# Optimization experiments

Hardware: AMD Instinct MI355X
Metric: run time of the kernel (lower is better)

## Reference

```python
import jax, jax.numpy as jnp
import numpy as np

B, S, D = 4, 2048, 1024


def setup_inputs() -> dict:
    key = jax.random.key(0)
    k1, k2, k3 = jax.random.split(key, 3)
    x = jax.random.normal(k1, (B, S, D), dtype=jnp.float32)
    # torch nn.Linear weights are [out_features, in_features]
    wq_w = jax.random.normal(k2, (D, D), dtype=jnp.float32) * (1.0 / np.sqrt(D))
    wv_w = jax.random.normal(k3, (D, D), dtype=jnp.float32) * (1.0 / np.sqrt(D))
    return {"x": x, "wq_w": wq_w, "wv_w": wv_w}


def reference(x, wq_w, wv_w):
    b, s, d = x.shape
    q = x @ wq_w.T                      # [B,S,D]
    kv = x @ wv_w.T                     # [B,S,D]  (original uses wv for BOTH k and v; wk unused)
    # original: k.view(B, k_dim, -1) -- a raw memory RESHAPE, not a transpose
    k_r = kv.reshape(b, d, s)           # [B,D,S]
    scores = jnp.einsum('bsd,bdt->bst', q, k_r) / np.sqrt(d)  # [B,S,S]
    sm = jax.nn.softmax(scores, axis=-1)
    sm = jnp.tril(sm)                   # post-softmax causal mask (rows NOT renormalized)
    return jnp.einsum('bst,btd->bsd', sm, kv)
```

## Files before the change

kernel.cpp:

```cpp
#include <hip/hip_runtime.h>


typedef __attribute__((ext_vector_type(8))) _Float16 f16x8;
typedef __attribute__((ext_vector_type(4))) _Float16 f16x4;
typedef __attribute__((ext_vector_type(4))) float f32x4;

__device__ __forceinline__ void glds16(const void* g, void* l) {
  __builtin_amdgcn_global_load_lds((const __attribute__((address_space(1))) void*)g,
                                   (__attribute__((address_space(3))) void*)l, 16, 0, 0);
}
#define BAR() __builtin_amdgcn_s_barrier()
#define LGKM0() do { asm volatile("s_waitcnt lgkmcnt(0)" ::: "memory"); \
                     __builtin_amdgcn_sched_barrier(0); } while (0)
#define VM2() asm volatile("s_waitcnt vmcnt(2)" ::: "memory")
#define VM0() asm volatile("s_waitcnt vmcnt(0)" ::: "memory")
#define PR1() __builtin_amdgcn_s_setprio(1)
#define PR0() __builtin_amdgcn_s_setprio(0)

__device__ __forceinline__ unsigned pkh2(float a, float b) {
  union { _Float16 h[2]; unsigned u; } c;
  c.h[0] = (_Float16)a; c.h[1] = (_Float16)b;
  return c.u;
}

__global__ __launch_bounds__(256) void cvt3(const float* __restrict__ x,
                                            const float* __restrict__ wq,
                                            const float* __restrict__ wv,
                                            _Float16* __restrict__ xh,
                                            _Float16* __restrict__ wqh,
                                            _Float16* __restrict__ wvh) {
  int i = blockIdx.x * 256 + threadIdx.x;
  const float* src;
  _Float16* dst;
  int off;
  if (i < 2097152) { src = x; dst = xh; off = i; }
  else if (i < 2359296) { src = wq; dst = wqh; off = i - 2097152; }
  else { src = wv; dst = wvh; off = i - 2359296; }
  float4 v = ((const float4*)src)[off];
  f16x4 o = {(_Float16)v.x, (_Float16)v.y, (_Float16)v.z, (_Float16)v.w};
  ((f16x4*)dst)[off] = o;
}

template <typename OUT_T, int EPI>
__global__ __launch_bounds__(512, 2) void gemm8p(const _Float16* __restrict__ A,
                                                 const _Float16* __restrict__ BT,
                                                 OUT_T* __restrict__ C,
                                                 _Float16* __restrict__ T1,
                                                 _Float16* __restrict__ T2,
                                                 int K, int ldc,
                                                 long sA, long sB, long sC, float scale,
                                                 int lgx, int lgy) {
  extern __shared__ char smem[];
  _Float16* lds = (_Float16*)smem;
  const int lin = blockIdx.x + gridDim.x * (blockIdx.y + gridDim.y * blockIdx.z);
  const int xcd = lin & 7, s = lin >> 3;
  const int G = (gridDim.y * gridDim.z) >> 3;
  const int mx = s & ((1 << lgx) - 1);
  const int pid = xcd * G + (s >> lgx);
  const int ny = pid & (gridDim.y - 1);
  const int bz = pid >> lgy;
  A += (size_t)bz * sA;
  BT += (size_t)bz * sB;
  C += (size_t)bz * sC;
  const int m0 = mx << 8, n0 = ny << 8;
  const int tid = threadIdx.x, lane = tid & 63, wave = tid >> 6;
  const int wm = wave >> 2, wn = wave & 3;
  const int lr = lane & 15, lk = lane >> 4, xr = lane & 7;
  const int nkt = K >> 6;
  const int A0 = 0, A1 = 8192, B0 = 16384, B1 = 24576, BUF = 32768;
  const int baseA = wm ? A1 : A0;
  const int baseB = B0 + ((wn >> 1) << 13);
  const int bRow = (wn & 1) << 6;
  const int srow = lane >> 3;
  const int scolB = ((lane & 7) << 4) ^ (srow << 4);

  f32x4 acc[8][4] = {};
  f16x8 fa[4][2], fb[4][2];

#define STAGE(bufsel, halfsel, G_, hrow0, kt) do {                                   \
    const _Float16* _g = (G_) + (size_t)((hrow0) + wave * 16 + srow) * K + ((kt) << 6); \
    glds16((const char*)_g + scolB, (char*)&lds[(bufsel) * BUF + (halfsel) + wave * 1024]); \
    glds16((const char*)(_g + (size_t)8 * K) + scolB,                                \
           (char*)&lds[(bufsel) * BUF + (halfsel) + wave * 1024 + 512]);             \
  } while (0)
#define RDA(buf, mf, ks) (*(const f16x8*)&lds[(buf) * BUF + baseA + ((mf) * 16 + lr) * 64 + \
                                              ((((ks) * 4 + lk) ^ xr) << 3)])
#define RDB(buf, nf, ks) (*(const f16x8*)&lds[(buf) * BUF + baseB + (bRow + (nf) * 16 + lr) * 64 + \
                                              ((((ks) * 4 + lk) ^ xr) << 3)])
#define RDFA4(b, mbase) do { _Pragma("unroll")                                        \
    for (int i = 0; i < 4; ++i) { fa[i][0] = RDA(b, (mbase) + i, 0);                  \
                                  fa[i][1] = RDA(b, (mbase) + i, 1); } } while (0)
#define RDFB2(b, jbase) do { _Pragma("unroll")                                        \
    for (int j = 0; j < 2; ++j) { fb[(jbase) + j][0] = RDB(b, (jbase) + j, 0);        \
                                  fb[(jbase) + j][1] = RDB(b, (jbase) + j, 1); } } while (0)
#define MMQ(ib, jb) do { _Pragma("unroll")                                            \
    for (int i = 0; i < 4; ++i) { _Pragma("unroll")                                   \
      for (int j = 0; j < 2; ++j) {                                                   \
        acc[(ib) + i][(jb) + j] = __builtin_amdgcn_mfma_f32_16x16x32_f16(             \
            fa[i][0], fb[(jb) + j][0], acc[(ib) + i][(jb) + j], 0, 0, 0);             \
        acc[(ib) + i][(jb) + j] = __builtin_amdgcn_mfma_f32_16x16x32_f16(             \
            fa[i][1], fb[(jb) + j][1], acc[(ib) + i][(jb) + j], 0, 0, 0);             \
      } } } while (0)

  STAGE(0, A0, A, m0, 0);
  STAGE(0, A1, A, m0 + 128, 0);
  STAGE(0, B0, BT, n0, 0);
  STAGE(0, B1, BT, n0 + 128, 0);
  STAGE(1, A0, A, m0, 1);
  VM2();
  BAR();

  for (int it = 0; it < (nkt >> 1); ++it) {
    const int t = it << 1;
    const int t2 = (t + 2 < nkt) ? t + 2 : 0;
    const int t3 = (t + 3 < nkt) ? t + 3 : 0;
    RDFA4(0, 0); RDFB2(0, 0);
    STAGE(1, A1, A, m0 + 128, t + 1);
    STAGE(1, B0, BT, n0, t + 1);
    BAR(); LGKM0(); PR1(); MMQ(0, 0); PR0(); BAR();
    RDFB2(0, 2);
    STAGE(1, B1, BT, n0 + 128, t + 1);
    BAR(); LGKM0(); PR1(); MMQ(0, 2); PR0(); BAR();
    RDFA4(0, 4);
    BAR(); LGKM0(); PR1(); MMQ(4, 2); PR0(); BAR();
    STAGE(0, A0, A, m0, t2);
    VM2();
    BAR(); PR1(); MMQ(4, 0); PR0(); BAR();
    RDFA4(1, 0); RDFB2(1, 0);
    STAGE(0, A1, A, m0 + 128, t2);
    STAGE(0, B0, BT, n0, t2);
    BAR(); LGKM0(); PR1(); MMQ(0, 0); PR0(); BAR();
    RDFB2(1, 2);
    STAGE(0, B1, BT, n0 + 128, t2);
    BAR(); LGKM0(); PR1(); MMQ(0, 2); PR0(); BAR();
    RDFA4(1, 4);
    BAR(); LGKM0(); PR1(); MMQ(4, 2); PR0(); BAR();
    STAGE(1, A0, A, m0, t3);
    VM2();
    BAR(); PR1(); MMQ(4, 0); PR0(); BAR();
  }

  if (EPI == 1 && bz == 1) {
    const int b = m0 >> 11;
    _Float16* kvvT = T1 + ((size_t)b << 21);
    _Float16* kvT  = T2 + ((size_t)b << 21);
    const int tb = (m0 & 2047) + wm * 128;
    const int db = n0 + wn * 64;
    char* wlds = smem + wave * 16384;
#pragma unroll
    for (int mf = 0; mf < 8; ++mf)
#pragma unroll
      for (int nf = 0; nf < 4; ++nf) {
        const int tl = mf * 16 + lk * 4;
        const int dl = nf * 16 + lr;
        const f32x4 a = acc[mf][nf];
        uint2 w = {pkh2(a[0], a[1]), pkh2(a[2], a[3])};
        *(uint2*)(wlds + dl * 256 + ((tl * 2) ^ ((dl & 7) << 4))) = w;
      }
#pragma unroll
    for (int it2 = 0; it2 < 32; ++it2) {
      const int dl = it2 * 2 + (lane >> 5);
      const int d = db + dl;
      const int tseg = (lane & 31) * 4;
      uint2 v = *(const uint2*)(wlds + dl * 256 + ((tseg * 2) ^ ((dl & 7) << 4)));
      *(uint2*)(kvT + (size_t)d * 2048 + tb + tseg) = v;
      unsigned ev = (v.x & 0xFFFFu) | (v.y << 16);
      unsigned od = (v.x >> 16) | (v.y & 0xFFFF0000u);
      const int k0 = (tb + tseg) >> 1;
      *(unsigned*)(kvvT + (size_t)d * 1024 + k0) = ev;
      *(unsigned*)(kvvT + (size_t)(1024 + d) * 1024 + k0) = od;
    }
  } else {
#pragma unroll
    for (int mf = 0; mf < 8; ++mf)
#pragma unroll
      for (int nf = 0; nf < 4; ++nf) {
        const int row = m0 + wm * 128 + mf * 16 + lk * 4;
        const int col = n0 + wn * 64 + nf * 16 + lr;
#pragma unroll
        for (int r = 0; r < 4; ++r)
          C[(size_t)(row + r) * ldc + col] = (OUT_T)(acc[mf][nf][r] * scale);
      }
  }
#undef STAGE
#undef RDA
#undef RDB
#undef RDFA4
#undef RDFB2
#undef MMQ
}

__global__ __launch_bounds__(256) void gemm_pv_bal(const _Float16* __restrict__ P,
                                                   const _Float16* __restrict__ KVT,
                                                   float* __restrict__ Out,
                                                   long sA, long sB, long sC) {
  __shared__ _Float16 As[2][64 * 64];
  __shared__ _Float16 Bs[2][128 * 64];
  const int total = gridDim.x * gridDim.y * gridDim.z;
  int lin = blockIdx.x + gridDim.x * (blockIdx.y + gridDim.y * blockIdx.z);
  const int xcd = lin & 7, slot = lin >> 3;
  const int perx = total >> 7;
  const int grp = xcd * perx + (slot >> 4);
  const int p = slot & 15;
  const int ny = grp & 7, bz = grp >> 3;
  P += (size_t)bz * sA;
  KVT += (size_t)bz * sB;
  Out += (size_t)bz * sC;
  const int n0 = ny * 128;
  const int lane = threadIdx.x & 63, wave = threadIdx.x >> 6;
  const int fr = lane & 15, lk = lane >> 4;
  const int srow = lane >> 3;
  const int scol = (((lane & 7) ^ srow) << 4);

#define PSTAGE(buf, m0s, t) do {                                                     \
    const int _k0 = (t) << 6;                                                        \
    _Pragma("unroll")                                                                \
    for (int c = 0; c < 2; ++c) {                                                    \
      const int ch = wave * 2 + c;                                                   \
      glds16((const char*)(P + (size_t)((m0s) + ch * 8 + srow) * 2048 + _k0) + scol, \
             &As[buf][ch * 512]);                                                    \
    }                                                                                \
    _Pragma("unroll")                                                                \
    for (int c = 0; c < 4; ++c) {                                                    \
      const int ch = wave * 4 + c;                                                   \
      glds16((const char*)(KVT + (size_t)(n0 + ch * 8 + srow) * 2048 + _k0) + scol,  \
             &Bs[buf][ch * 512]);                                                    \
    }                                                                                \
  } while (0)

#pragma unroll
  for (int half = 0; half < 2; ++half) {
    const int strip = half ? (31 - p) : p;
    const int m0s = strip * 64;
    const int nt = strip + 1;
    f32x4 acc[4][2] = {};
    PSTAGE(0, m0s, 0);
    VM0();
    BAR();
    for (int t = 0; t < nt; ++t) {
      const int cur = t & 1;
      if (t + 1 < nt) PSTAGE(cur ^ 1, m0s, t + 1);
      f16x8 af[4][2], bf[2][2];
#pragma unroll
      for (int m = 0; m < 4; ++m) {
        const int r = m * 16 + fr;
#pragma unroll
        for (int ks = 0; ks < 2; ++ks)
          af[m][ks] = *(const f16x8*)&As[cur][r * 64 + (((ks * 4 + lk) ^ (r & 7)) << 3)];
      }
#pragma unroll
      for (int n = 0; n < 2; ++n) {
        const int rb = wave * 32 + n * 16 + fr;
#pragma unroll
        for (int ks = 0; ks < 2; ++ks)
          bf[n][ks] = *(const f16x8*)&Bs[cur][rb * 64 + (((ks * 4 + lk) ^ (rb & 7)) << 3)];
      }
      LGKM0();
      PR1();
#pragma unroll
      for (int ks = 0; ks < 2; ++ks)
#pragma unroll
        for (int m = 0; m < 4; ++m)
#pragma unroll
          for (int n = 0; n < 2; ++n)
            acc[m][n] = __builtin_amdgcn_mfma_f32_16x16x32_f16(af[m][ks], bf[n][ks],
                                                               acc[m][n], 0, 0, 0);
      PR0();
      VM0();
      BAR();
    }
#pragma unroll
    for (int m = 0; m < 4; ++m)
#pragma unroll
      for (int n = 0; n < 2; ++n) {
        const int row = m0s + m * 16 + lk * 4;
        const int col = n0 + wave * 32 + n * 16 + fr;
#pragma unroll
        for (int r = 0; r < 4; ++r)
          Out[(size_t)(row + r) * 1024 + col] = acc[m][n][r];
      }
  }
#undef PSTAGE
}

__global__ __launch_bounds__(256) void softmax_mask(_Float16* __restrict__ S) {
  const int row = blockIdx.x;
  const int s = row & 2047;
  _Float16* p = S + (size_t)row * 2048;
  const int tid = threadIdx.x;
  uint4 u = ((const uint4*)p)[tid];
  const _Float16* h = (const _Float16*)&u;
  float v[8];
#pragma unroll
  for (int j = 0; j < 8; ++j) v[j] = (float)h[j];
  float mx = v[0];
#pragma unroll
  for (int j = 1; j < 8; ++j) mx = fmaxf(mx, v[j]);
#pragma unroll
  for (int off = 32; off > 0; off >>= 1) mx = fmaxf(mx, __shfl_xor(mx, off));
  __shared__ float red[8];
  const int wave = tid >> 6, lane = tid & 63;
  if (lane == 0) red[wave] = mx;
  __syncthreads();
  mx = fmaxf(fmaxf(red[0], red[1]), fmaxf(red[2], red[3]));
  float se = 0.f;
#pragma unroll
  for (int j = 0; j < 8; ++j) se += __expf(v[j] - mx);
#pragma unroll
  for (int off = 32; off > 0; off >>= 1) se += __shfl_xor(se, off);
  if (lane == 0) red[4 + wave] = se;
  __syncthreads();
  const float inv = 1.f / (red[4] + red[5] + red[6] + red[7]);
  const int lim = (s & ~63) + 64;
  if (tid * 8 < lim) {
    _Float16 o[8];
#pragma unroll
    for (int j = 0; j < 8; ++j) {
      int t = tid * 8 + j;
      o[j] = (_Float16)((t <= s) ? __expf(v[j] - mx) * inv : 0.f);
    }
    ((uint4*)p)[tid] = *(const uint4*)o;
  }
}

extern "C" void kernel_launch(void* const* d_in, const int* in_sizes, int n_in,
                              void* d_out, int out_size, void* d_ws, size_t ws_size,
                              hipStream_t stream) {
  const float* x = (const float*)d_in[0];
  const float* wq = (const float*)d_in[1];
  const float* wv = (const float*)d_in[2];
  float* out = (float*)d_out;
  char* ws = (char*)d_ws;

  const size_t MB = 1024 * 1024;
  const int bc = (ws_size >= 85 * MB) ? 4 : 2;
  const size_t scBytes = (size_t)bc * 2048 * 2048 * 2;
  const long PB = 2048 * 1024;
  const long SB = (long)2048 * 2048;

  _Float16* Sc = (_Float16*)ws;
  _Float16* qh = (_Float16*)(ws + scBytes);
  _Float16* kvvT = (_Float16*)(ws + scBytes + 16 * MB);
  _Float16* kvT = (_Float16*)(ws + scBytes + 32 * MB);
  _Float16* wqh = (_Float16*)(ws + scBytes + 48 * MB);
  _Float16* wvh = (_Float16*)(ws + scBytes + 50 * MB);
  _Float16* xh = (_Float16*)ws;

  cvt3<<<10240, 256, 0, stream>>>(x, wq, wv, xh, wqh, wvh);

  gemm8p<_Float16, 1><<<dim3(32, 4, 2), 512, 131072, stream>>>(
      xh, wqh, qh, kvvT, kvT, 1024, 1024, 0, (long)(wvh - wqh), 0, 1.0f, 5, 2);

  for (int b0 = 0; b0 < 4; b0 += bc) {
    gemm8p<_Float16, 0><<<dim3(8, 8, bc), 512, 131072, stream>>>(
        qh + (size_t)b0 * PB, kvvT + (size_t)b0 * PB, Sc, nullptr, nullptr,
        1024, 2048, PB, PB, SB, 0.03125f, 3, 3);
    softmax_mask<<<bc * 2048, 256, 0, stream>>>(Sc);
    gemm_pv_bal<<<dim3(16, 8, bc), 256, 0, stream>>>(
        Sc, kvT + (size_t)b0 * PB, out + (size_t)b0 * PB, SB, PB, PB);
  }
}
```

Measured before the change: 136.0 us.

## Fuse softmax stats into QK GEMM epilogue and normalize inside PV GEMM

```diff
diff --git a/kernel.cpp b/kernel.cpp
--- a/kernel.cpp
+++ b/kernel.cpp
@@ -14,6 +14,7 @@
                      __builtin_amdgcn_sched_barrier(0); } while (0)
 #define VM2() asm volatile("s_waitcnt vmcnt(2)" ::: "memory")
 #define VM0() asm volatile("s_waitcnt vmcnt(0)" ::: "memory")
+#define VMLG0() asm volatile("s_waitcnt vmcnt(0) lgkmcnt(0)" ::: "memory")
 #define PR1() __builtin_amdgcn_s_setprio(1)
 #define PR0() __builtin_amdgcn_s_setprio(0)
 
@@ -170,6 +171,41 @@
       *(unsigned*)(kvvT + (size_t)d * 1024 + k0) = ev;
       *(unsigned*)(kvvT + (size_t)(1024 + d) * 1024 + k0) = od;
     }
+  } else if (EPI == 2) {
+    float2* Pst = (float2*)T1 + (size_t)bz * 2048 * 32;
+    const int gidx = (n0 >> 6) + wn;
+#pragma unroll
+    for (int mf = 0; mf < 8; ++mf)
+#pragma unroll
+      for (int r = 0; r < 4; ++r) {
+        float v0 = acc[mf][0][r] * scale;
+        float v1 = acc[mf][1][r] * scale;
+        float v2 = acc[mf][2][r] * scale;
+        float v3 = acc[mf][3][r] * scale;
+        float mxv = fmaxf(fmaxf(v0, v1), fmaxf(v2, v3));
+#pragma unroll
+        for (int off = 1; off < 16; off <<= 1) mxv = fmaxf(mxv, __shfl_xor(mxv, off));
+        float sm = __expf(v0 - mxv) + __expf(v1 - mxv) +
+                   __expf(v2 - mxv) + __expf(v3 - mxv);
+#pragma unroll
+        for (int off = 1; off < 16; off <<= 1) sm += __shfl_xor(sm, off);
+        if (lr == 0) {
+          const int row = m0 + wm * 128 + mf * 16 + lk * 4 + r;
+          Pst[(size_t)row * 32 + gidx] = make_float2(mxv, sm);
+        }
+      }
+    if (n0 <= m0) {
+#pragma unroll
+      for (int mf = 0; mf < 8; ++mf)
+#pragma unroll
+        for (int nf = 0; nf < 4; ++nf) {
+          const int row = m0 + wm * 128 + mf * 16 + lk * 4;
+          const int col = n0 + wn * 64 + nf * 16 + lr;
+#pragma unroll
+          for (int r = 0; r < 4; ++r)
+            C[(size_t)(row + r) * ldc + col] = (OUT_T)(acc[mf][nf][r] * scale);
+        }
+    }
   } else {
 #pragma unroll
     for (int mf = 0; mf < 8; ++mf)
@@ -190,8 +226,22 @@
 #undef MMQ
 }
 
+__global__ __launch_bounds__(256) void stats_combine(const float2* __restrict__ Pst,
+                                                     float2* __restrict__ St) {
+  const int row = blockIdx.x * 256 + threadIdx.x;
+  const float2* p = Pst + (size_t)row * 32;
+  float m = -1e30f;
+#pragma unroll
+  for (int g = 0; g < 32; ++g) m = fmaxf(m, p[g].x);
+  float l = 0.f;
+#pragma unroll
+  for (int g = 0; g < 32; ++g) { float2 t = p[g]; l += t.y * __expf(t.x - m); }
+  St[row] = make_float2(m, 1.f / l);
+}
+
 __global__ __launch_bounds__(256) void gemm_pv_bal(const _Float16* __restrict__ P,
                                                    const _Float16* __restrict__ KVT,
+                                                   const float2* __restrict__ St,
                                                    float* __restrict__ Out,
                                                    long sA, long sB, long sC) {
   __shared__ _Float16 As[2][64 * 64];
@@ -206,20 +256,16 @@
   P += (size_t)bz * sA;
   KVT += (size_t)bz * sB;
   Out += (size_t)bz * sC;
+  St += (size_t)bz * 2048;
   const int n0 = ny * 128;
   const int lane = threadIdx.x & 63, wave = threadIdx.x >> 6;
   const int fr = lane & 15, lk = lane >> 4;
   const int srow = lane >> 3;
-  const int scol = (((lane & 7) ^ srow) << 4);
-
-#define PSTAGE(buf, m0s, t) do {                                                     \
+  const int q = lane & 7;
+  const int scol = ((q ^ srow) << 4);
+
+#define BSTAGE(buf, t) do {                                                          \
     const int _k0 = (t) << 6;                                                        \
-    _Pragma("unroll")                                                                \
-    for (int c = 0; c < 2; ++c) {                                                    \
-      const int ch = wave * 2 + c;                                                   \
-      glds16((const char*)(P + (size_t)((m0s) + ch * 8 + srow) * 2048 + _k0) + scol, \
-             &As[buf][ch * 512]);                                                    \
-    }                                                                                \
     _Pragma("unroll")                                                                \
     for (int c = 0; c < 4; ++c) {                                                    \
       const int ch = wave * 4 + c;                                                   \
@@ -227,19 +273,48 @@
              &Bs[buf][ch * 512]);                                                    \
     }                                                                                \
   } while (0)
+#define ALOAD(t) do {                                                                \
+    const size_t _kb = ((size_t)(t) << 6) + q * 8;                                   \
+    a0 = *(const uint4*)(P + (size_t)rowL0 * 2048 + _kb);                            \
+    a1 = *(const uint4*)(P + (size_t)rowL1 * 2048 + _kb);                            \
+  } while (0)
+#define AXF(buf, t) do {                                                             \
+    const int _kb = ((t) << 6) + q * 8;                                              \
+    const _Float16* h0 = (const _Float16*)&a0;                                       \
+    const _Float16* h1 = (const _Float16*)&a1;                                       \
+    _Float16 o0[8], o1[8];                                                           \
+    _Pragma("unroll")                                                                \
+    for (int j = 0; j < 8; ++j) {                                                    \
+      const int col = _kb + j;                                                       \
+      float p0 = __expf((float)h0[j] - mS0) * ilS0;                                  \
+      float p1 = __expf((float)h1[j] - mS1) * ilS1;                                  \
+      o0[j] = (_Float16)((col <= rowL0) ? p0 : 0.f);                                 \
+      o1[j] = (_Float16)((col <= rowL1) ? p1 : 0.f);                                 \
+    }                                                                                \
+    char* base_ = (char*)&As[buf][0];                                                \
+    *(uint4*)(base_ + (wave * 2 + 0) * 1024 + srow * 128 + scol) = *(const uint4*)o0; \
+    *(uint4*)(base_ + (wave * 2 + 1) * 1024 + srow * 128 + scol) = *(const uint4*)o1; \
+  } while (0)
 
 #pragma unroll
   for (int half = 0; half < 2; ++half) {
     const int strip = half ? (31 - p) : p;
     const int m0s = strip * 64;
     const int nt = strip + 1;
+    const int rowL0 = m0s + (wave * 2) * 8 + srow;
+    const int rowL1 = rowL0 + 8;
+    const float2 st0 = St[rowL0], st1 = St[rowL1];
+    const float mS0 = st0.x, ilS0 = st0.y, mS1 = st1.x, ilS1 = st1.y;
+    uint4 a0, a1;
     f32x4 acc[4][2] = {};
-    PSTAGE(0, m0s, 0);
-    VM0();
+    ALOAD(0);
+    BSTAGE(0, 0);
+    AXF(0, 0);
+    VMLG0();
     BAR();
     for (int t = 0; t < nt; ++t) {
       const int cur = t & 1;
-      if (t + 1 < nt) PSTAGE(cur ^ 1, m0s, t + 1);
+      if (t + 1 < nt) { BSTAGE(cur ^ 1, t + 1); ALOAD(t + 1); }
       f16x8 af[4][2], bf[2][2];
 #pragma unroll
       for (int m = 0; m < 4; ++m) {
@@ -266,7 +341,8 @@
             acc[m][n] = __builtin_amdgcn_mfma_f32_16x16x32_f16(af[m][ks], bf[n][ks],
                                                                acc[m][n], 0, 0, 0);
       PR0();
-      VM0();
+      if (t + 1 < nt) { AXF(cur ^ 1, t + 1); }
+      VMLG0();
       BAR();
     }
 #pragma unroll
@@ -280,47 +356,9 @@
           Out[(size_t)(row + r) * 1024 + col] = acc[m][n][r];
       }
   }
-#undef PSTAGE
-}
-
-__global__ __launch_bounds__(256) void softmax_mask(_Float16* __restrict__ S) {
-  const int row = blockIdx.x;
-  const int s = row & 2047;
-  _Float16* p = S + (size_t)row * 2048;
-  const int tid = threadIdx.x;
-  uint4 u = ((const uint4*)p)[tid];
-  const _Float16* h = (const _Float16*)&u;
-  float v[8];
-#pragma unroll
-  for (int j = 0; j < 8; ++j) v[j] = (float)h[j];
-  float mx = v[0];
-#pragma unroll
-  for (int j = 1; j < 8; ++j) mx = fmaxf(mx, v[j]);
-#pragma unroll
-  for (int off = 32; off > 0; off >>= 1) mx = fmaxf(mx, __shfl_xor(mx, off));
-  __shared__ float red[8];
-  const int wave = tid >> 6, lane = tid & 63;
-  if (lane == 0) red[wave] = mx;
-  __syncthreads();
-  mx = fmaxf(fmaxf(red[0], red[1]), fmaxf(red[2], red[3]));
-  float se = 0.f;
-#pragma unroll
-  for (int j = 0; j < 8; ++j) se += __expf(v[j] - mx);
-#pragma unroll
-  for (int off = 32; off > 0; off >>= 1) se += __shfl_xor(se, off);
-  if (lane == 0) red[4 + wave] = se;
-  __syncthreads();
-  const float inv = 1.f / (red[4] + red[5] + red[6] + red[7]);
-  const int lim = (s & ~63) + 64;
-  if (tid * 8 < lim) {
-    _Float16 o[8];
-#pragma unroll
-    for (int j = 0; j < 8; ++j) {
-      int t = tid * 8 + j;
-      o[j] = (_Float16)((t <= s) ? __expf(v[j] - mx) * inv : 0.f);
-    }
-    ((uint4*)p)[tid] = *(const uint4*)o;
-  }
+#undef BSTAGE
+#undef ALOAD
+#undef AXF
 }
 
 extern "C" void kernel_launch(void* const* d_in, const int* in_sizes, int n_in,
@@ -333,7 +371,7 @@
   char* ws = (char*)d_ws;
 
   const size_t MB = 1024 * 1024;
-  const int bc = (ws_size >= 85 * MB) ? 4 : 2;
+  const int bc = (ws_size >= 88 * MB) ? 4 : 2;
   const size_t scBytes = (size_t)bc * 2048 * 2048 * 2;
   const long PB = 2048 * 1024;
   const long SB = (long)2048 * 2048;
@@ -344,6 +382,8 @@
   _Float16* kvT = (_Float16*)(ws + scBytes + 32 * MB);
   _Float16* wqh = (_Float16*)(ws + scBytes + 48 * MB);
   _Float16* wvh = (_Float16*)(ws + scBytes + 50 * MB);
+  float2* Pst = (float2*)(ws + scBytes + 52 * MB);
+  float2* Stt = (float2*)(ws + scBytes + 54 * MB);
   _Float16* xh = (_Float16*)ws;
 
   cvt3<<<10240, 256, 0, stream>>>(x, wq, wv, xh, wqh, wvh);
@@ -352,11 +392,11 @@
       xh, wqh, qh, kvvT, kvT, 1024, 1024, 0, (long)(wvh - wqh), 0, 1.0f, 5, 2);
 
   for (int b0 = 0; b0 < 4; b0 += bc) {
-    gemm8p<_Float16, 0><<<dim3(8, 8, bc), 512, 131072, stream>>>(
-        qh + (size_t)b0 * PB, kvvT + (size_t)b0 * PB, Sc, nullptr, nullptr,
+    gemm8p<_Float16, 2><<<dim3(8, 8, bc), 512, 131072, stream>>>(
+        qh + (size_t)b0 * PB, kvvT + (size_t)b0 * PB, Sc, (_Float16*)Pst, nullptr,
         1024, 2048, PB, PB, SB, 0.03125f, 3, 3);
-    softmax_mask<<<bc * 2048, 256, 0, stream>>>(Sc);
+    stats_combine<<<bc * 8, 256, 0, stream>>>(Pst, Stt);
     gemm_pv_bal<<<dim3(16, 8, bc), 256, 0, stream>>>(
-        Sc, kvT + (size_t)b0 * PB, out + (size_t)b0 * PB, SB, PB, PB);
+        Sc, kvT + (size_t)b0 * PB, Stt, out + (size_t)b0 * PB, SB, PB, PB);
   }
 }
```

Result: slower. 149.6 us (+10.0%).
